# Kernel tuning notes

Measured on AMD Instinct MI355X. Metric: run time of the kernel, lower is better.

## Reference

```python
import jax, jax.numpy as jnp
import numpy as np

N_KERNELS = 11
INV_SQRT_2PI = 1.0 / np.sqrt(2.0 * 3.141592653589793)


def kernel_mus(n_kernels):
    l_mu = [1.0]
    if n_kernels == 1:
        return l_mu
    bin_size = 2.0 / (n_kernels - 1)
    l_mu.append(1 - bin_size / 2)
    for i in range(1, n_kernels - 1):
        l_mu.append(l_mu[i] - bin_size)
    return l_mu


def kernel_sigmas(n_kernels):
    bin_size = 2.0 / (n_kernels - 1)
    l_sigma = [0.0001]
    if n_kernels == 1:
        return l_sigma
    l_sigma += [0.5 * bin_size] * (n_kernels - 1)
    return l_sigma


MU = jnp.asarray(kernel_mus(N_KERNELS), dtype=jnp.float32)        # [K]
SIGMA = jnp.asarray(kernel_sigmas(N_KERNELS), dtype=jnp.float32)  # [K]


def setup_inputs() -> dict:
    key = jax.random.key(0)
    k1, k2, k3, k4 = jax.random.split(key, 4)
    B, Q, D, V, E = 512, 32, 256, 32000, 128
    return {
        "query_tokens": jax.random.randint(k1, (B, Q), 0, V),
        "doc_tokens": jax.random.randint(k2, (B, D), 0, V),
        "embedding": jax.random.normal(k3, (V, E), dtype=jnp.float32),
        "fc_weight": jax.random.normal(k4, (1, N_KERNELS), dtype=jnp.float32) * 0.3,
    }


def reference(query_tokens, doc_tokens, embedding, fc_weight):
    # embedding lookup + L2 normalization along feature dim
    q_emb = embedding[query_tokens]                                  # [B,Q,E]
    d_emb = embedding[doc_tokens]                                    # [B,D,E]
    q_n = q_emb / jnp.linalg.norm(q_emb, axis=-1, keepdims=True)
    d_n = d_emb / jnp.linalg.norm(d_emb, axis=-1, keepdims=True)

    # cosine similarity translation matrix [B,Q,D]
    tm = jnp.einsum("bqe,bde->bqd", q_n, d_n)

    # Gaussian kernel responses [B,Q,D,K] (vectorized over kernels)
    diff = tm[..., None] - MU                                        # [B,Q,D,K]
    kmat = jnp.exp(-(diff * diff) / (2.0 * SIGMA * SIGMA)) * INV_SQRT_2PI

    # masking: pad/OOV tokens (id 0) masked out
    q_mask = (query_tokens > 0).astype(jnp.float32)                  # [B,Q]
    d_mask = (doc_tokens > 0).astype(jnp.float32)                    # [B,D]
    kmat = kmat * q_mask[:, :, None, None] * d_mask[:, None, :, None]

    # kernel pooling: sum over doc, log, masked sum over query
    per_kernel_query = jnp.sum(kmat, axis=2)                         # [B,Q,K]
    log_pool = jnp.log(jnp.clip(per_kernel_query, 1e-10)) * q_mask[:, :, None]
    per_kernel = jnp.sum(log_pool, axis=1)                           # [B,K]

    # final linear (no bias) -> score per (query, document) pair
    return jnp.squeeze(per_kernel @ fc_weight.T, axis=-1)            # [B]
```

## Files before the change

kernel.cpp:

```cpp
#include <hip/hip_runtime.h>
#include <hip/hip_bf16.h>

#define VOCAB 32000
#define EDIM  128
#define QN    32
#define DN    256
#define NK    11

typedef __attribute__((ext_vector_type(8))) short bf16x8;
typedef __attribute__((ext_vector_type(4))) float f32x4;

#define EXP2F(x) __builtin_amdgcn_exp2f(x)

template <int CTRL>
static __device__ inline float dpp_add(float x) {
    int y = __builtin_amdgcn_update_dpp(0, __float_as_int(x), CTRL, 0xF, 0xF, true);
    return x + __int_as_float(y);
}
static __device__ inline float sum16(float x) {
    x = dpp_add<0xB1>(x);
    x = dpp_add<0x4E>(x);
    x = dpp_add<0x124>(x);
    x = dpp_add<0x128>(x);
    return x;
}

static __device__ inline int swz(int r, int c) { return c ^ ((r & 7) << 4); }

static __device__ inline bf16x8 pack8(float4 a, float4 b) {
    union { bf16x8 v; __hip_bfloat16 h[8]; } u;
    u.h[0] = __float2bfloat16(a.x); u.h[1] = __float2bfloat16(a.y);
    u.h[2] = __float2bfloat16(a.z); u.h[3] = __float2bfloat16(a.w);
    u.h[4] = __float2bfloat16(b.x); u.h[5] = __float2bfloat16(b.y);
    u.h[6] = __float2bfloat16(b.z); u.h[7] = __float2bfloat16(b.w);
    return u.v;
}

__global__ __launch_bounds__(512, 2) void knrm_fused(const int* __restrict__ qtok,
                                                     const int* __restrict__ dtok,
                                                     const float* __restrict__ emb,
                                                     const float* __restrict__ fcw,
                                                     float* __restrict__ out) {
    __shared__ __align__(16) unsigned short dbuf[DN * EDIM];
    __shared__ __align__(16) unsigned short qbuf[QN * EDIM];
    __shared__ int   dtokS[DN];
    __shared__ int   qtokS[QN];
    __shared__ float invS[DN + QN];
    __shared__ float redS[8];

    const float INV_SQRT_2PI = 0.3989422804014327f;
    const float CCH[9] = {8886110.5f, 162754.797f, 2980.95799f, 54.5981500f, 1.0f,
                          0.0183156389f, 3.35462628e-4f, 6.14421235e-6f, 1.12535175e-7f};

    int b = blockIdx.x, tid = threadIdx.x;
    int w = tid >> 6, lane = tid & 63;
    int lr = lane & 15, lg = lane >> 4;

    if (tid < DN) dtokS[tid] = dtok[b * DN + tid];
    else if (tid < DN + QN) qtokS[tid - DN] = qtok[b * QN + (tid - DN)];
    __syncthreads();

    {
        int j = lr, sub = lg;
        {
            int qr = (w << 2) + sub;
            int tok = qtokS[qr];
            const float4* src = (const float4*)(emb + (size_t)tok * EDIM) + j * 2;
            float4 v0 = src[0], v1 = src[1];
            float ss = v0.x * v0.x + v0.y * v0.y + v0.z * v0.z + v0.w * v0.w;
            ss = fmaf(v1.x, v1.x, ss); ss = fmaf(v1.y, v1.y, ss);
            ss = fmaf(v1.z, v1.z, ss); ss = fmaf(v1.w, v1.w, ss);
            float tot = sum16(ss);
            if (j == 0) invS[DN + qr] = 1.0f / sqrtf(tot);
            *(bf16x8*)((char*)qbuf + qr * 256 + swz(qr, j * 16)) = pack8(v0, v1);
        }
        #pragma unroll
        for (int it = 0; it < 8; ++it) {
            int r = (w << 5) + (it << 2) + sub;
            int tok = dtokS[r];
            const float4* src = (const float4*)(emb + (size_t)tok * EDIM) + j * 2;
            float4 v0 = src[0], v1 = src[1];
            float ss = v0.x * v0.x + v0.y * v0.y + v0.z * v0.z + v0.w * v0.w;
            ss = fmaf(v1.x, v1.x, ss); ss = fmaf(v1.y, v1.y, ss);
            ss = fmaf(v1.z, v1.z, ss); ss = fmaf(v1.w, v1.w, ss);
            float tot = sum16(ss);
            if (j == 0) invS[r] = 1.0f / sqrtf(tot);
            *(bf16x8*)((char*)dbuf + r * 256 + swz(r, j * 16)) = pack8(v0, v1);
        }
    }
    __syncthreads();

    int qt = w & 1, ds = w >> 1;

    bf16x8 A0, A1, A2, A3;
    {
        int qr = (qt << 4) + lr;
        const char* qb = (const char*)qbuf + qr * 256;
        A0 = *(const bf16x8*)(qb + swz(qr, lg * 16));
        A1 = *(const bf16x8*)(qb + swz(qr, lg * 16 + 64));
        A2 = *(const bf16x8*)(qb + swz(qr, lg * 16 + 128));
        A3 = *(const bf16x8*)(qb + swz(qr, lg * 16 + 192));
    }
    int   qtr[4];
    float invq[4];
    #pragma unroll
    for (int r = 0; r < 4; ++r) {
        int qrow = (qt << 4) + (lg << 2) + r;
        qtr[r]  = qtokS[qrow];
        invq[r] = invS[DN + qrow];
    }
    __syncthreads();

    float* part = (float*)qbuf;

    float kacc[4][NK];
    #pragma unroll
    for (int r = 0; r < 4; ++r)
        #pragma unroll
        for (int k = 0; k < NK; ++k) kacc[r][k] = 0.0f;

    #pragma unroll
    for (int t = 0; t < 4; ++t) {
        int dr = (ds << 6) + (t << 4) + lr;
        const char* db = (const char*)dbuf + dr * 256;
        bf16x8 B0 = *(const bf16x8*)(db + swz(dr, lg * 16));
        bf16x8 B1 = *(const bf16x8*)(db + swz(dr, lg * 16 + 64));
        bf16x8 B2 = *(const bf16x8*)(db + swz(dr, lg * 16 + 128));
        bf16x8 B3 = *(const bf16x8*)(db + swz(dr, lg * 16 + 192));
        int   tcur = dtokS[dr];
        float invd = invS[dr];

        f32x4 acc = {0.0f, 0.0f, 0.0f, 0.0f};
        acc = __builtin_amdgcn_mfma_f32_16x16x32_bf16(A0, B0, acc, 0, 0, 0);
        acc = __builtin_amdgcn_mfma_f32_16x16x32_bf16(A1, B1, acc, 0, 0, 0);
        acc = __builtin_amdgcn_mfma_f32_16x16x32_bf16(A2, B2, acc, 0, 0, 0);
        acc = __builtin_amdgcn_mfma_f32_16x16x32_bf16(A3, B3, acc, 0, 0, 0);

        float sc = (tcur > 0) ? INV_SQRT_2PI : 0.0f;
        #pragma unroll
        for (int r = 0; r < 4; ++r) {
            float t2 = acc[r] * (invq[r] * invd);
            kacc[r][0] += (tcur == qtr[r]) ? sc : 0.0f;
            float s   = fabsf(t2);
            float scP = (t2 >= 0.0f) ? sc : 0.0f;
            float scN = sc - scP;
            float d   = s - 0.9f;
            float g   = EXP2F(d * d * -72.1347520f);
            float E   = EXP2F(s * -28.8539008f);
            #pragma unroll
            for (int m = 1; m <= 10; ++m) {
                kacc[r][m]      = fmaf(g, scP, kacc[r][m]);
                kacc[r][11 - m] = fmaf(g, scN, kacc[r][11 - m]);
                if (m < 10) g = g * E * CCH[m - 1];
            }
        }
    }

    #pragma unroll
    for (int r = 0; r < 4; ++r)
        #pragma unroll
        for (int k = 0; k < NK; ++k) kacc[r][k] = sum16(kacc[r][k]);

    if (lr == 0) {
        float* pw = part + w * (16 * NK) + (lg * 4) * NK;
        #pragma unroll
        for (int r = 0; r < 4; ++r)
            #pragma unroll
            for (int k = 0; k < NK; ++k)
                pw[r * NK + k] = kacc[r][k];
    }
    __syncthreads();

    float total = 0.0f;
    if (tid < QN * NK) {
        int q = tid / NK, k = tid - (tid / NK) * NK;
        int qt2 = q >> 4, row = q & 15;
        const float* pb = part + qt2 * (16 * NK) + row * NK + k;
        float v = pb[0] + pb[2 * 16 * NK] + pb[4 * 16 * NK] + pb[6 * 16 * NK];
        float m = (qtokS[q] > 0) ? 1.0f : 0.0f;
        total = m * fcw[k] * __logf(fmaxf(v, 1e-10f));
    }
    #pragma unroll
    for (int off = 32; off; off >>= 1) total += __shfl_xor(total, off);
    if (lane == 0) redS[w] = total;
    __syncthreads();
    if (tid == 0) {
        float s = 0.0f;
        #pragma unroll
        for (int i = 0; i < 8; ++i) s += redS[i];
        out[b] = s;
    }
}

extern "C" void kernel_launch(void* const* d_in, const int* in_sizes, int n_in,
                              void* d_out, int out_size, void* d_ws, size_t ws_size,
                              hipStream_t stream) {
    const int*   qtok = (const int*)d_in[0];
    const int*   dtok = (const int*)d_in[1];
    const float* emb  = (const float*)d_in[2];
    const float* fcw  = (const float*)d_in[3];
    float* out = (float*)d_out;

    int B = in_sizes[0] / QN;
    knrm_fused<<<B, 512, 0, stream>>>(qtok, dtok, emb, fcw, out);
}
```

Measured before the change: 23.58 us.

## Software-pipeline embedding gathers and LDS B-tile loads; raise launch-bounds occupancy hint

```diff
diff --git a/kernel.cpp b/kernel.cpp
--- a/kernel.cpp
+++ b/kernel.cpp
@@ -35,8 +35,14 @@
     u.h[6] = __float2bfloat16(b.z); u.h[7] = __float2bfloat16(b.w);
     return u.v;
 }
-
-__global__ __launch_bounds__(512, 2) void knrm_fused(const int* __restrict__ qtok,
+static __device__ inline float dot8(float4 a, float4 b) {
+    float s = a.x * a.x + a.y * a.y + a.z * a.z + a.w * a.w;
+    s = fmaf(b.x, b.x, s); s = fmaf(b.y, b.y, s);
+    s = fmaf(b.z, b.z, s); s = fmaf(b.w, b.w, s);
+    return s;
+}
+
+__global__ __launch_bounds__(512, 4) void knrm_fused(const int* __restrict__ qtok,
                                                      const int* __restrict__ dtok,
                                                      const float* __restrict__ emb,
                                                      const float* __restrict__ fcw,
@@ -61,32 +67,51 @@
     __syncthreads();
 
     {
-        int j = lr, sub = lg;
-        {
-            int qr = (w << 2) + sub;
-            int tok = qtokS[qr];
-            const float4* src = (const float4*)(emb + (size_t)tok * EDIM) + j * 2;
-            float4 v0 = src[0], v1 = src[1];
-            float ss = v0.x * v0.x + v0.y * v0.y + v0.z * v0.z + v0.w * v0.w;
-            ss = fmaf(v1.x, v1.x, ss); ss = fmaf(v1.y, v1.y, ss);
-            ss = fmaf(v1.z, v1.z, ss); ss = fmaf(v1.w, v1.w, ss);
-            float tot = sum16(ss);
-            if (j == 0) invS[DN + qr] = 1.0f / sqrtf(tot);
-            *(bf16x8*)((char*)qbuf + qr * 256 + swz(qr, j * 16)) = pack8(v0, v1);
+        float ss[9];
+        float4 La[3][2], Lb[3][2];
+
+        #define ROWID(slot) ((slot) == 0 ? (DN + (w << 2) + lg) \
+                                         : ((w << 5) + (((slot) - 1) << 2) + lg))
+        #define TOKOF(rid)  ((rid) >= DN ? qtokS[(rid) - DN] : dtokS[(rid)])
+
+        #define CHUNK_LOAD(Larr, c)                                              \
+            _Pragma("unroll")                                                    \
+            for (int s = 0; s < 3; ++s) {                                        \
+                int rid = ROWID((c) * 3 + s);                                    \
+                int tok = TOKOF(rid);                                            \
+                const float4* src = (const float4*)(emb + (size_t)tok * EDIM) + lr * 2; \
+                Larr[s][0] = src[0];                                             \
+                Larr[s][1] = src[1];                                             \
+            }
+
+        #define CHUNK_PROC(Larr, c)                                              \
+            _Pragma("unroll")                                                    \
+            for (int s = 0; s < 3; ++s) {                                        \
+                int slot = (c) * 3 + s;                                          \
+                int rid = ROWID(slot);                                           \
+                char* base = (rid >= DN) ? (char*)qbuf + (rid - DN) * 256        \
+                                         : (char*)dbuf + rid * 256;              \
+                *(bf16x8*)(base + swz(rid, lr * 16)) = pack8(Larr[s][0], Larr[s][1]); \
+                ss[slot] = dot8(Larr[s][0], Larr[s][1]);                         \
+            }
+
+        CHUNK_LOAD(La, 0)
+        CHUNK_LOAD(Lb, 1)
+        CHUNK_PROC(La, 0)
+        CHUNK_LOAD(La, 2)
+        CHUNK_PROC(Lb, 1)
+        CHUNK_PROC(La, 2)
+
+        #pragma unroll
+        for (int slot = 0; slot < 9; ++slot) {
+            int rid = ROWID(slot);
+            float tot = sum16(ss[slot]);
+            if (lr == 0) invS[rid] = 1.0f / sqrtf(tot);
         }
-        #pragma unroll
-        for (int it = 0; it < 8; ++it) {
-            int r = (w << 5) + (it << 2) + sub;
-            int tok = dtokS[r];
-            const float4* src = (const float4*)(emb + (size_t)tok * EDIM) + j * 2;
-            float4 v0 = src[0], v1 = src[1];
-            float ss = v0.x * v0.x + v0.y * v0.y + v0.z * v0.z + v0.w * v0.w;
-            ss = fmaf(v1.x, v1.x, ss); ss = fmaf(v1.y, v1.y, ss);
-            ss = fmaf(v1.z, v1.z, ss); ss = fmaf(v1.w, v1.w, ss);
-            float tot = sum16(ss);
-            if (j == 0) invS[r] = 1.0f / sqrtf(tot);
-            *(bf16x8*)((char*)dbuf + r * 256 + swz(r, j * 16)) = pack8(v0, v1);
-        }
+        #undef CHUNK_LOAD
+        #undef CHUNK_PROC
+        #undef ROWID
+        #undef TOKOF
     }
     __syncthreads();
 
@@ -119,22 +144,37 @@
         #pragma unroll
         for (int k = 0; k < NK; ++k) kacc[r][k] = 0.0f;
 
+    bf16x8 Bc0, Bc1, Bc2, Bc3;
+    {
+        int dr = (ds << 6) + lr;
+        const char* db = (const char*)dbuf + dr * 256;
+        Bc0 = *(const bf16x8*)(db + swz(dr, lg * 16));
+        Bc1 = *(const bf16x8*)(db + swz(dr, lg * 16 + 64));
+        Bc2 = *(const bf16x8*)(db + swz(dr, lg * 16 + 128));
+        Bc3 = *(const bf16x8*)(db + swz(dr, lg * 16 + 192));
+    }
+
     #pragma unroll
     for (int t = 0; t < 4; ++t) {
         int dr = (ds << 6) + (t << 4) + lr;
-        const char* db = (const char*)dbuf + dr * 256;
-        bf16x8 B0 = *(const bf16x8*)(db + swz(dr, lg * 16));
-        bf16x8 B1 = *(const bf16x8*)(db + swz(dr, lg * 16 + 64));
-        bf16x8 B2 = *(const bf16x8*)(db + swz(dr, lg * 16 + 128));
-        bf16x8 B3 = *(const bf16x8*)(db + swz(dr, lg * 16 + 192));
-        int   tcur = dtokS[dr];
+        int tcur = dtokS[dr];
         float invd = invS[dr];
 
+        bf16x8 Bn0, Bn1, Bn2, Bn3;
+        if (t < 3) {
+            int drn = dr + 16;
+            const char* db = (const char*)dbuf + drn * 256;
+            Bn0 = *(const bf16x8*)(db + swz(drn, lg * 16));
+            Bn1 = *(const bf16x8*)(db + swz(drn, lg * 16 + 64));
+            Bn2 = *(const bf16x8*)(db + swz(drn, lg * 16 + 128));
+            Bn3 = *(const bf16x8*)(db + swz(drn, lg * 16 + 192));
+        }
+
         f32x4 acc = {0.0f, 0.0f, 0.0f, 0.0f};
-        acc = __builtin_amdgcn_mfma_f32_16x16x32_bf16(A0, B0, acc, 0, 0, 0);
-        acc = __builtin_amdgcn_mfma_f32_16x16x32_bf16(A1, B1, acc, 0, 0, 0);
-        acc = __builtin_amdgcn_mfma_f32_16x16x32_bf16(A2, B2, acc, 0, 0, 0);
-        acc = __builtin_amdgcn_mfma_f32_16x16x32_bf16(A3, B3, acc, 0, 0, 0);
+        acc = __builtin_amdgcn_mfma_f32_16x16x32_bf16(A0, Bc0, acc, 0, 0, 0);
+        acc = __builtin_amdgcn_mfma_f32_16x16x32_bf16(A1, Bc1, acc, 0, 0, 0);
+        acc = __builtin_amdgcn_mfma_f32_16x16x32_bf16(A2, Bc2, acc, 0, 0, 0);
+        acc = __builtin_amdgcn_mfma_f32_16x16x32_bf16(A3, Bc3, acc, 0, 0, 0);
 
         float sc = (tcur > 0) ? INV_SQRT_2PI : 0.0f;
         #pragma unroll
@@ -154,6 +194,8 @@
                 if (m < 10) g = g * E * CCH[m - 1];
             }
         }
+
+        Bc0 = Bn0; Bc1 = Bn1; Bc2 = Bn2; Bc3 = Bn3;
     }
 
     #pragma unroll
```

New measurement: 24.51 us. +3.9%, slower.

## Split each batch row across two blocks over doc halves with separate reduce kernel

Applied to the files above, without the earlier changes.

```diff
diff --git a/kernel.cpp b/kernel.cpp
--- a/kernel.cpp
+++ b/kernel.cpp
@@ -1,10 +1,10 @@
 #include <hip/hip_runtime.h>
 #include <hip/hip_bf16.h>
 
-#define VOCAB 32000
 #define EDIM  128
 #define QN    32
 #define DN    256
+#define DH    128
 #define NK    11
 
 typedef __attribute__((ext_vector_type(8))) short bf16x8;
@@ -35,83 +35,76 @@
     u.h[6] = __float2bfloat16(b.z); u.h[7] = __float2bfloat16(b.w);
     return u.v;
 }
-
-__global__ __launch_bounds__(512, 2) void knrm_fused(const int* __restrict__ qtok,
-                                                     const int* __restrict__ dtok,
-                                                     const float* __restrict__ emb,
-                                                     const float* __restrict__ fcw,
-                                                     float* __restrict__ out) {
-    __shared__ __align__(16) unsigned short dbuf[DN * EDIM];
-    __shared__ __align__(16) unsigned short qbuf[QN * EDIM];
-    __shared__ int   dtokS[DN];
+static __device__ inline float sumsq8(float4 a, float4 b) {
+    float s = a.x * a.x + a.y * a.y + a.z * a.z + a.w * a.w;
+    s = fmaf(b.x, b.x, s); s = fmaf(b.y, b.y, s);
+    s = fmaf(b.z, b.z, s); s = fmaf(b.w, b.w, s);
+    return s;
+}
+
+__global__ __launch_bounds__(512, 6) void knrm_half(const int* __restrict__ qtok,
+                                                    const int* __restrict__ dtok,
+                                                    const float* __restrict__ emb,
+                                                    float* __restrict__ part) {
+    __shared__ __align__(16) unsigned short dbuf[DH * EDIM];
+    __shared__ int   dtokS[DH];
     __shared__ int   qtokS[QN];
-    __shared__ float invS[DN + QN];
-    __shared__ float redS[8];
+    __shared__ float invS[DH];
 
     const float INV_SQRT_2PI = 0.3989422804014327f;
-    const float CCH[9] = {8886110.5f, 162754.797f, 2980.95799f, 54.5981500f, 1.0f,
-                          0.0183156389f, 3.35462628e-4f, 6.14421235e-6f, 1.12535175e-7f};
-
-    int b = blockIdx.x, tid = threadIdx.x;
+
+    int bid = blockIdx.x;
+    int b = bid >> 1, h = bid & 1;
+    int tid = threadIdx.x;
     int w = tid >> 6, lane = tid & 63;
     int lr = lane & 15, lg = lane >> 4;
 
-    if (tid < DN) dtokS[tid] = dtok[b * DN + tid];
-    else if (tid < DN + QN) qtokS[tid - DN] = qtok[b * QN + (tid - DN)];
-    __syncthreads();
-
+    if (tid < DH) dtokS[tid] = dtok[b * DN + h * DH + tid];
+    else if (tid < DH + QN) qtokS[tid - DH] = qtok[b * QN + (tid - DH)];
+    __syncthreads();
+
+    int qt = w & 1, ds = w >> 1;
+
+    float4 qv[4][2];
     {
-        int j = lr, sub = lg;
-        {
-            int qr = (w << 2) + sub;
-            int tok = qtokS[qr];
-            const float4* src = (const float4*)(emb + (size_t)tok * EDIM) + j * 2;
-            float4 v0 = src[0], v1 = src[1];
-            float ss = v0.x * v0.x + v0.y * v0.y + v0.z * v0.z + v0.w * v0.w;
-            ss = fmaf(v1.x, v1.x, ss); ss = fmaf(v1.y, v1.y, ss);
-            ss = fmaf(v1.z, v1.z, ss); ss = fmaf(v1.w, v1.w, ss);
-            float tot = sum16(ss);
-            if (j == 0) invS[DN + qr] = 1.0f / sqrtf(tot);
-            *(bf16x8*)((char*)qbuf + qr * 256 + swz(qr, j * 16)) = pack8(v0, v1);
+        int tok = qtokS[(qt << 4) + lr];
+        const float4* src = (const float4*)(emb + (size_t)tok * EDIM);
+        #pragma unroll
+        for (int s = 0; s < 4; ++s) {
+            qv[s][0] = src[lg * 2 + s * 8];
+            qv[s][1] = src[lg * 2 + s * 8 + 1];
         }
-        #pragma unroll
-        for (int it = 0; it < 8; ++it) {
-            int r = (w << 5) + (it << 2) + sub;
-            int tok = dtokS[r];
-            const float4* src = (const float4*)(emb + (size_t)tok * EDIM) + j * 2;
-            float4 v0 = src[0], v1 = src[1];
-            float ss = v0.x * v0.x + v0.y * v0.y + v0.z * v0.z + v0.w * v0.w;
-            ss = fmaf(v1.x, v1.x, ss); ss = fmaf(v1.y, v1.y, ss);
-            ss = fmaf(v1.z, v1.z, ss); ss = fmaf(v1.w, v1.w, ss);
-            float tot = sum16(ss);
-            if (j == 0) invS[r] = 1.0f / sqrtf(tot);
-            *(bf16x8*)((char*)dbuf + r * 256 + swz(r, j * 16)) = pack8(v0, v1);
-        }
-    }
-    __syncthreads();
-
-    int qt = w & 1, ds = w >> 1;
-
-    bf16x8 A0, A1, A2, A3;
-    {
-        int qr = (qt << 4) + lr;
-        const char* qb = (const char*)qbuf + qr * 256;
-        A0 = *(const bf16x8*)(qb + swz(qr, lg * 16));
-        A1 = *(const bf16x8*)(qb + swz(qr, lg * 16 + 64));
-        A2 = *(const bf16x8*)(qb + swz(qr, lg * 16 + 128));
-        A3 = *(const bf16x8*)(qb + swz(qr, lg * 16 + 192));
-    }
+    }
+
+    #pragma unroll
+    for (int it = 0; it < 4; ++it) {
+        int r = (w << 4) + (it << 2) + lg;
+        int tok = dtokS[r];
+        const float4* src = (const float4*)(emb + (size_t)tok * EDIM) + lr * 2;
+        float4 v0 = src[0], v1 = src[1];
+        float tot = sum16(sumsq8(v0, v1));
+        if (lr == 0) invS[r] = 1.0f / sqrtf(tot);
+        *(bf16x8*)((char*)dbuf + r * 256 + swz(r, lr * 16)) = pack8(v0, v1);
+    }
+
+    float ssq = sumsq8(qv[0][0], qv[0][1]) + sumsq8(qv[1][0], qv[1][1]) +
+                sumsq8(qv[2][0], qv[2][1]) + sumsq8(qv[3][0], qv[3][1]);
+    ssq += __shfl_xor(ssq, 16);
+    ssq += __shfl_xor(ssq, 32);
+    float myinv = 1.0f / sqrtf(ssq);
+    float invq[4];
     int   qtr[4];
-    float invq[4];
     #pragma unroll
     for (int r = 0; r < 4; ++r) {
-        int qrow = (qt << 4) + (lg << 2) + r;
-        qtr[r]  = qtokS[qrow];
-        invq[r] = invS[DN + qrow];
-    }
-    __syncthreads();
-
-    float* part = (float*)qbuf;
+        invq[r] = __shfl(myinv, lg * 20 + r);
+        qtr[r]  = qtokS[(qt << 4) + (lg << 2) + r];
+    }
+    bf16x8 A0 = pack8(qv[0][0], qv[0][1]);
+    bf16x8 A1 = pack8(qv[1][0], qv[1][1]);
+    bf16x8 A2 = pack8(qv[2][0], qv[2][1]);
+    bf16x8 A3 = pack8(qv[3][0], qv[3][1]);
+
+    __syncthreads();
 
     float kacc[4][NK];
     #pragma unroll
@@ -119,14 +112,16 @@
         #pragma unroll
         for (int k = 0; k < NK; ++k) kacc[r][k] = 0.0f;
 
-    #pragma unroll
-    for (int t = 0; t < 4; ++t) {
-        int dr = (ds << 6) + (t << 4) + lr;
+    int xr = (lr & 7) << 4;
+
+    #pragma unroll
+    for (int t = 0; t < 2; ++t) {
+        int dr = (ds << 5) + (t << 4) + lr;
         const char* db = (const char*)dbuf + dr * 256;
-        bf16x8 B0 = *(const bf16x8*)(db + swz(dr, lg * 16));
-        bf16x8 B1 = *(const bf16x8*)(db + swz(dr, lg * 16 + 64));
-        bf16x8 B2 = *(const bf16x8*)(db + swz(dr, lg * 16 + 128));
-        bf16x8 B3 = *(const bf16x8*)(db + swz(dr, lg * 16 + 192));
+        bf16x8 B0 = *(const bf16x8*)(db + ((lg * 16      ) ^ xr));
+        bf16x8 B1 = *(const bf16x8*)(db + ((lg * 16 +  64) ^ xr));
+        bf16x8 B2 = *(const bf16x8*)(db + ((lg * 16 + 128) ^ xr));
+        bf16x8 B3 = *(const bf16x8*)(db + ((lg * 16 + 192) ^ xr));
         int   tcur = dtokS[dr];
         float invd = invS[dr];
 
@@ -141,18 +136,29 @@
         for (int r = 0; r < 4; ++r) {
             float t2 = acc[r] * (invq[r] * invd);
             kacc[r][0] += (tcur == qtr[r]) ? sc : 0.0f;
-            float s   = fabsf(t2);
-            float scP = (t2 >= 0.0f) ? sc : 0.0f;
-            float scN = sc - scP;
-            float d   = s - 0.9f;
-            float g   = EXP2F(d * d * -72.1347520f);
-            float E   = EXP2F(s * -28.8539008f);
-            #pragma unroll
-            for (int m = 1; m <= 10; ++m) {
-                kacc[r][m]      = fmaf(g, scP, kacc[r][m]);
-                kacc[r][11 - m] = fmaf(g, scN, kacc[r][11 - m]);
-                if (m < 10) g = g * E * CCH[m - 1];
-            }
+            float d  = t2 - 0.1f;
+            float g  = EXP2F(d * d * -72.1347520f);
+            float Em = EXP2F(t2 * -28.8539008f);
+            float Ep = EXP2F(t2 *  28.8539008f);
+            kacc[r][5] = fmaf(g, sc, kacc[r][5]);
+            float gd = g * Em;
+            kacc[r][6] = fmaf(gd, sc, kacc[r][6]);
+            gd = gd * Em * 0.0183156389f;
+            kacc[r][7] = fmaf(gd, sc, kacc[r][7]);
+            gd = gd * Em * 3.35462628e-4f;
+            kacc[r][8] = fmaf(gd, sc, kacc[r][8]);
+            gd = gd * Em * 6.14421235e-6f;
+            kacc[r][9] = fmaf(gd, sc, kacc[r][9]);
+            gd = gd * Em * 1.12535175e-7f;
+            kacc[r][10] = fmaf(gd, sc, kacc[r][10]);
+            float gu = g * Ep * 0.0183156389f;
+            kacc[r][4] = fmaf(gu, sc, kacc[r][4]);
+            gu = gu * Ep * 3.35462628e-4f;
+            kacc[r][3] = fmaf(gu, sc, kacc[r][3]);
+            gu = gu * Ep * 6.14421235e-6f;
+            kacc[r][2] = fmaf(gu, sc, kacc[r][2]);
+            gu = gu * Ep * 1.12535175e-7f;
+            kacc[r][1] = fmaf(gu, sc, kacc[r][1]);
         }
     }
 
@@ -161,8 +167,10 @@
         #pragma unroll
         for (int k = 0; k < NK; ++k) kacc[r][k] = sum16(kacc[r][k]);
 
+    __syncthreads();
+    float* partS = (float*)dbuf;
     if (lr == 0) {
-        float* pw = part + w * (16 * NK) + (lg * 4) * NK;
+        float* pw = partS + (w * 16 + (lg << 2)) * NK;
         #pragma unroll
         for (int r = 0; r < 4; ++r)
             #pragma unroll
@@ -171,25 +179,40 @@
     }
     __syncthreads();
 
-    float total = 0.0f;
-    if (tid < QN * NK) {
-        int q = tid / NK, k = tid - (tid / NK) * NK;
+    if (tid < 2 * 16 * NK) {
+        int q = tid / NK;
+        int k = tid - q * NK;
         int qt2 = q >> 4, row = q & 15;
-        const float* pb = part + qt2 * (16 * NK) + row * NK + k;
-        float v = pb[0] + pb[2 * 16 * NK] + pb[4 * 16 * NK] + pb[6 * 16 * NK];
-        float m = (qtokS[q] > 0) ? 1.0f : 0.0f;
-        total = m * fcw[k] * __logf(fmaxf(v, 1e-10f));
-    }
-    #pragma unroll
-    for (int off = 32; off; off >>= 1) total += __shfl_xor(total, off);
-    if (lane == 0) redS[w] = total;
-    __syncthreads();
-    if (tid == 0) {
-        float s = 0.0f;
-        #pragma unroll
-        for (int i = 0; i < 8; ++i) s += redS[i];
-        out[b] = s;
-    }
+        float v = 0.0f;
+        #pragma unroll
+        for (int d2 = 0; d2 < 4; ++d2)
+            v += partS[(((d2 << 1) | qt2) * 16 + row) * NK + k];
+        part[(size_t)bid * (QN * NK) + tid] = v;
+    }
+}
+
+__global__ __launch_bounds__(128) void knrm_reduce(const int* __restrict__ qtok,
+                                                   const float* __restrict__ part,
+                                                   const float* __restrict__ fcw,
+                                                   float* __restrict__ out) {
+    __shared__ float red[2];
+    int b = blockIdx.x, tid = threadIdx.x;
+    const float* p0 = part + (size_t)(b * 2) * (QN * NK);
+    const float* p1 = p0 + QN * NK;
+
+    float sum = 0.0f;
+    for (int i = tid; i < QN * NK; i += 128) {
+        int q = i / NK;
+        int k = i - q * NK;
+        float v = p0[i] + p1[i];
+        float m = (qtok[b * QN + q] > 0) ? 1.0f : 0.0f;
+        sum += m * fcw[k] * __logf(fmaxf(v, 1e-10f));
+    }
+    #pragma unroll
+    for (int off = 32; off; off >>= 1) sum += __shfl_xor(sum, off);
+    if ((tid & 63) == 0) red[tid >> 6] = sum;
+    __syncthreads();
+    if (tid == 0) out[b] = red[0] + red[1];
 }
 
 extern "C" void kernel_launch(void* const* d_in, const int* in_sizes, int n_in,
@@ -199,8 +222,10 @@
     const int*   dtok = (const int*)d_in[1];
     const float* emb  = (const float*)d_in[2];
     const float* fcw  = (const float*)d_in[3];
-    float* out = (float*)d_out;
+    float* out  = (float*)d_out;
+    float* part = (float*)d_ws;
 
     int B = in_sizes[0] / QN;
-    knrm_fused<<<B, 512, 0, stream>>>(qtok, dtok, emb, fcw, out);
-}
+    knrm_half<<<B * 2, 512, 0, stream>>>(qtok, dtok, emb, part);
+    knrm_reduce<<<B, 128, 0, stream>>>(qtok, part, fcw, out);
+}
```

Result: slower. 34.39 us (+45.8%).

## Overlap second-half doc embedding gather with first-half MFMA and kernel pooling

Applied to the files above, without the earlier changes.

```diff
diff --git a/kernel.cpp b/kernel.cpp
--- a/kernel.cpp
+++ b/kernel.cpp
@@ -1,7 +1,6 @@
 #include <hip/hip_runtime.h>
 #include <hip/hip_bf16.h>
 
-#define VOCAB 32000
 #define EDIM  128
 #define QN    32
 #define DN    256
@@ -35,8 +34,14 @@
     u.h[6] = __float2bfloat16(b.z); u.h[7] = __float2bfloat16(b.w);
     return u.v;
 }
-
-__global__ __launch_bounds__(512, 2) void knrm_fused(const int* __restrict__ qtok,
+static __device__ inline float sumsq8(float4 a, float4 b) {
+    float s = a.x * a.x + a.y * a.y + a.z * a.z + a.w * a.w;
+    s = fmaf(b.x, b.x, s); s = fmaf(b.y, b.y, s);
+    s = fmaf(b.z, b.z, s); s = fmaf(b.w, b.w, s);
+    return s;
+}
+
+__global__ __launch_bounds__(512, 4) void knrm_fused(const int* __restrict__ qtok,
                                                      const int* __restrict__ dtok,
                                                      const float* __restrict__ emb,
                                                      const float* __restrict__ fcw,
@@ -48,9 +53,11 @@
     __shared__ float invS[DN + QN];
     __shared__ float redS[8];
 
-    const float INV_SQRT_2PI = 0.3989422804014327f;
-    const float CCH[9] = {8886110.5f, 162754.797f, 2980.95799f, 54.5981500f, 1.0f,
-                          0.0183156389f, 3.35462628e-4f, 6.14421235e-6f, 1.12535175e-7f};
+    const float C0 = 0.3989422804014327f;
+    const float C1 = 7.30620157e-3f;
+    const float C2 = 2.45119242e-6f;
+    const float C3 = 1.50605972e-11f;
+    const float C4 = 1.69484929e-18f;
 
     int b = blockIdx.x, tid = threadIdx.x;
     int w = tid >> 6, lane = tid & 63;
@@ -61,32 +68,23 @@
     __syncthreads();
 
     {
-        int j = lr, sub = lg;
-        {
-            int qr = (w << 2) + sub;
-            int tok = qtokS[qr];
-            const float4* src = (const float4*)(emb + (size_t)tok * EDIM) + j * 2;
-            float4 v0 = src[0], v1 = src[1];
-            float ss = v0.x * v0.x + v0.y * v0.y + v0.z * v0.z + v0.w * v0.w;
-            ss = fmaf(v1.x, v1.x, ss); ss = fmaf(v1.y, v1.y, ss);
-            ss = fmaf(v1.z, v1.z, ss); ss = fmaf(v1.w, v1.w, ss);
-            float tot = sum16(ss);
-            if (j == 0) invS[DN + qr] = 1.0f / sqrtf(tot);
-            *(bf16x8*)((char*)qbuf + qr * 256 + swz(qr, j * 16)) = pack8(v0, v1);
-        }
-        #pragma unroll
-        for (int it = 0; it < 8; ++it) {
-            int r = (w << 5) + (it << 2) + sub;
-            int tok = dtokS[r];
-            const float4* src = (const float4*)(emb + (size_t)tok * EDIM) + j * 2;
-            float4 v0 = src[0], v1 = src[1];
-            float ss = v0.x * v0.x + v0.y * v0.y + v0.z * v0.z + v0.w * v0.w;
-            ss = fmaf(v1.x, v1.x, ss); ss = fmaf(v1.y, v1.y, ss);
-            ss = fmaf(v1.z, v1.z, ss); ss = fmaf(v1.w, v1.w, ss);
-            float tot = sum16(ss);
-            if (j == 0) invS[r] = 1.0f / sqrtf(tot);
-            *(bf16x8*)((char*)dbuf + r * 256 + swz(r, j * 16)) = pack8(v0, v1);
-        }
+        int qr = (w << 2) + lg;
+        int tok = qtokS[qr];
+        const float4* src = (const float4*)(emb + (size_t)tok * EDIM) + lr * 2;
+        float4 v0 = src[0], v1 = src[1];
+        float tot = sum16(sumsq8(v0, v1));
+        if (lr == 0) invS[DN + qr] = 1.0f / sqrtf(tot);
+        *(bf16x8*)((char*)qbuf + qr * 256 + swz(qr, lr * 16)) = pack8(v0, v1);
+    }
+    #pragma unroll
+    for (int it = 0; it < 4; ++it) {
+        int r = (w << 4) + (it << 2) + lg;
+        int tok = dtokS[r];
+        const float4* src = (const float4*)(emb + (size_t)tok * EDIM) + lr * 2;
+        float4 v0 = src[0], v1 = src[1];
+        float tot = sum16(sumsq8(v0, v1));
+        if (lr == 0) invS[r] = 1.0f / sqrtf(tot);
+        *(bf16x8*)((char*)dbuf + r * 256 + swz(r, lr * 16)) = pack8(v0, v1);
     }
     __syncthreads();
 
@@ -109,9 +107,6 @@
         qtr[r]  = qtokS[qrow];
         invq[r] = invS[DN + qrow];
     }
-    __syncthreads();
-
-    float* part = (float*)qbuf;
 
     float kacc[4][NK];
     #pragma unroll
@@ -119,9 +114,8 @@
         #pragma unroll
         for (int k = 0; k < NK; ++k) kacc[r][k] = 0.0f;
 
-    #pragma unroll
-    for (int t = 0; t < 4; ++t) {
-        int dr = (ds << 6) + (t << 4) + lr;
+    auto evalTile = [&](int t) {
+        int dr = (t << 6) + (ds << 4) + lr;
         const char* db = (const char*)dbuf + dr * 256;
         bf16x8 B0 = *(const bf16x8*)(db + swz(dr, lg * 16));
         bf16x8 B1 = *(const bf16x8*)(db + swz(dr, lg * 16 + 64));
@@ -136,31 +130,55 @@
         acc = __builtin_amdgcn_mfma_f32_16x16x32_bf16(A2, B2, acc, 0, 0, 0);
         acc = __builtin_amdgcn_mfma_f32_16x16x32_bf16(A3, B3, acc, 0, 0, 0);
 
-        float sc = (tcur > 0) ? INV_SQRT_2PI : 0.0f;
+        bool dok = (tcur > 0);
+        float mc = dok ? C0 : 0.0f;
         #pragma unroll
         for (int r = 0; r < 4; ++r) {
             float t2 = acc[r] * (invq[r] * invd);
-            kacc[r][0] += (tcur == qtr[r]) ? sc : 0.0f;
-            float s   = fabsf(t2);
-            float scP = (t2 >= 0.0f) ? sc : 0.0f;
-            float scN = sc - scP;
-            float d   = s - 0.9f;
-            float g   = EXP2F(d * d * -72.1347520f);
-            float E   = EXP2F(s * -28.8539008f);
-            #pragma unroll
-            for (int m = 1; m <= 10; ++m) {
-                kacc[r][m]      = fmaf(g, scP, kacc[r][m]);
-                kacc[r][11 - m] = fmaf(g, scN, kacc[r][11 - m]);
-                if (m < 10) g = g * E * CCH[m - 1];
-            }
+            kacc[r][0] += (tcur == qtr[r]) ? mc : 0.0f;
+            float d  = t2 - 0.1f;
+            float g  = EXP2F(d * d * -72.1347520f);
+            g = dok ? g : 0.0f;
+            float Em = EXP2F(t2 * -28.8539008f);
+            float Ep = EXP2F(t2 *  28.8539008f);
+            float h = g;
+            kacc[r][5]  += h * C0;
+            h *= Em; kacc[r][6]  += h * C0;
+            h *= Em; kacc[r][7]  += h * C1;
+            h *= Em; kacc[r][8]  += h * C2;
+            h *= Em; kacc[r][9]  += h * C3;
+            h *= Em; kacc[r][10] += h * C4;
+            h = g;
+            h *= Ep; kacc[r][4]  += h * C1;
+            h *= Ep; kacc[r][3]  += h * C2;
+            h *= Ep; kacc[r][2]  += h * C3;
+            h *= Ep; kacc[r][1]  += h * C4;
         }
-    }
+    };
+
+    #pragma unroll
+    for (int it = 0; it < 4; ++it) {
+        int r = 128 + (w << 4) + (it << 2) + lg;
+        int tok = dtokS[r];
+        const float4* src = (const float4*)(emb + (size_t)tok * EDIM) + lr * 2;
+        float4 v0 = src[0], v1 = src[1];
+        float tot = sum16(sumsq8(v0, v1));
+        if (lr == 0) invS[r] = 1.0f / sqrtf(tot);
+        *(bf16x8*)((char*)dbuf + r * 256 + swz(r, lr * 16)) = pack8(v0, v1);
+    }
+    evalTile(0);
+    evalTile(1);
+    __syncthreads();
+
+    evalTile(2);
+    evalTile(3);
 
     #pragma unroll
     for (int r = 0; r < 4; ++r)
         #pragma unroll
         for (int k = 0; k < NK; ++k) kacc[r][k] = sum16(kacc[r][k]);
 
+    float* part = (float*)qbuf;
     if (lr == 0) {
         float* pw = part + w * (16 * NK) + (lg * 4) * NK;
         #pragma unroll
```

Result: faster. 21.21 us (median of 2 runs) (-10.1%).
